# Optimization experiments

Hardware: AMD Instinct MI355X
Metric: run time of the kernel (lower is better)

The kernel has to match this reference:

```python
import jax, jax.numpy as jnp
import numpy as np

N, E, F_IN, F_HID, F_OUT = 50000, 800000, 128, 128, 64


def setup_inputs() -> dict:
    key = jax.random.key(0)
    k_x, k_e, k_w1, k_w2 = jax.random.split(key, 4)
    x = jax.random.normal(k_x, (N, F_IN), dtype=jnp.float32)
    edge_index = jax.random.randint(k_e, (2, E), 0, N, dtype=jnp.int32)
    # GCNConv params (glorot-ish scale)
    W1 = jax.random.normal(k_w1, (F_IN, F_HID), dtype=jnp.float32) * (1.0 / np.sqrt(F_IN))
    b1 = jnp.zeros((F_HID,), dtype=jnp.float32)
    W2 = jax.random.normal(k_w2, (F_HID, F_OUT), dtype=jnp.float32) * (1.0 / np.sqrt(F_HID))
    b2 = jnp.zeros((F_OUT,), dtype=jnp.float32)
    return {"x": x, "edge_index": edge_index, "W1": W1, "b1": b1, "W2": W2, "b2": b2}


def reference(x, edge_index, W1, b1, W2, b2):
    n = x.shape[0]
    # PyG GCNConv: add self-loops, symmetric normalization deg^-1/2 * deg^-1/2
    loops = jnp.arange(n, dtype=edge_index.dtype)
    src = jnp.concatenate([edge_index[0], loops])  # (E+N,)
    dst = jnp.concatenate([edge_index[1], loops])  # (E+N,)
    deg = jax.ops.segment_sum(jnp.ones_like(dst, dtype=x.dtype), dst, num_segments=n)
    dinv = jnp.where(deg > 0, jax.lax.rsqrt(jnp.maximum(deg, 1.0)), 0.0)
    norm = dinv[src] * dinv[dst]  # (E+N,)

    def conv(h, W, b):
        h = h @ W                               # (n, f_out)
        msg = h[src] * norm[:, None]            # gather + scale, (E+N, f_out)
        return jax.ops.segment_sum(msg, dst, num_segments=n) + b

    h = jax.nn.relu(conv(x, W1, b1))  # dropout p=0.0 -> identity
    return conv(h, W2, b2)
```

## Files before the change

### kernel.cpp

```cpp
#include <hip/hip_runtime.h>

typedef __bf16 bf16x8 __attribute__((ext_vector_type(8)));
typedef float  f32x4  __attribute__((ext_vector_type(4)));

__device__ __forceinline__ float bf2f(unsigned short h) {
    return __uint_as_float(((unsigned int)h) << 16);
}
__device__ __forceinline__ unsigned short f2bf(float f) {
    unsigned int u = __float_as_uint(f);
    u += 0x7FFFu + ((u >> 16) & 1u);
    return (unsigned short)(u >> 16);
}
__device__ __forceinline__ void unpack8(uint4 u, float* v) {
    v[0] = __uint_as_float(u.x << 16); v[1] = __uint_as_float(u.x & 0xFFFF0000u);
    v[2] = __uint_as_float(u.y << 16); v[3] = __uint_as_float(u.y & 0xFFFF0000u);
    v[4] = __uint_as_float(u.z << 16); v[5] = __uint_as_float(u.z & 0xFFFF0000u);
    v[6] = __uint_as_float(u.w << 16); v[7] = __uint_as_float(u.w & 0xFFFF0000u);
}

__global__ void k1_deg_detect(const int* __restrict__ dst, int* __restrict__ deg,
                              int* __restrict__ rank, int E,
                              const unsigned short* __restrict__ x, int* __restrict__ cnt,
                              int degBlocks) {
    if ((int)blockIdx.x < degBlocks) {
        int base = blockIdx.x * 1024 + threadIdx.x;
#pragma unroll
        for (int k = 0; k < 4; ++k) {
            int e = base + k * 256;
            if (e < E) rank[e] = atomicAdd(&deg[dst[e]], 1);
        }
    } else {
        int c = 0;
        for (int i = threadIdx.x; i < 4096; i += 256) {
            unsigned e = (x[i] >> 7) & 0xFFu;
            if (e >= 0x88u) ++c;
        }
        if (c) atomicAdd(cnt, c);
    }
}

template <int COLS>
__device__ __forceinline__ void prepack_one(const void* W, unsigned short* Wp, int idx,
                                            bool isf32) {
    if (idx >= (COLS / 16) * 4 * 64) return;
    int lane = idx & 63;
    int ks   = (idx >> 6) & 3;
    int nt   = idx >> 8;
    int col  = nt * 16 + (lane & 15);
    int krow = ks * 32 + (lane >> 4) * 8;
    unsigned short tmp[8];
#pragma unroll
    for (int j = 0; j < 8; ++j) {
        size_t e = (size_t)(krow + j) * COLS + col;
        float v = isf32 ? ((const float*)W)[e] : bf2f(((const unsigned short*)W)[e]);
        tmp[j] = f2bf(v);
    }
    *(uint4*)(Wp + (size_t)idx * 8) = *(uint4*)tmp;
}

__global__ void k2_scan1_prep(const int* __restrict__ deg, int* __restrict__ offs,
                              int* __restrict__ bsum, float* __restrict__ dinv, int N, int NB,
                              const void* __restrict__ W1, const void* __restrict__ W2,
                              const void* __restrict__ b1, const void* __restrict__ b2,
                              unsigned short* __restrict__ Wp1, unsigned short* __restrict__ Wp2,
                              float* __restrict__ b1f, float* __restrict__ b2f,
                              const int* __restrict__ cnt) {
    __shared__ int s[256];
    int t = threadIdx.x;
    if ((int)blockIdx.x < NB) {
        int base = blockIdx.x * 1024 + t * 4;
        int d4[4];
#pragma unroll
        for (int k = 0; k < 4; ++k) d4[k] = (base + k < N) ? deg[base + k] : 0;
#pragma unroll
        for (int k = 0; k < 4; ++k)
            if (base + k < N) dinv[base + k] = rsqrtf((float)d4[k] + 1.0f);
        int mySum = d4[0] + d4[1] + d4[2] + d4[3];
        s[t] = mySum;
        __syncthreads();
        for (int d = 1; d < 256; d <<= 1) {
            int v = (t >= d) ? s[t - d] : 0;
            __syncthreads();
            s[t] += v;
            __syncthreads();
        }
        int run = s[t] - mySum;
#pragma unroll
        for (int k = 0; k < 4; ++k) {
            if (base + k < N) offs[base + k] = run;
            run += d4[k];
        }
        if (t == 255) bsum[blockIdx.x] = s[255];
    } else {
        bool isf32 = (*cnt >= 16);
        int bid = blockIdx.x - NB;
        if (bid < 8) {
            prepack_one<128>(W1, Wp1, bid * 256 + t, isf32);
        } else if (bid < 12) {
            prepack_one<64>(W2, Wp2, (bid - 8) * 256 + t, isf32);
        } else {
            if (t < 128) b1f[t] = isf32 ? ((const float*)b1)[t]
                                        : bf2f(((const unsigned short*)b1)[t]);
            else if (t < 192) b2f[t - 128] = isf32 ? ((const float*)b2)[t - 128]
                                                   : bf2f(((const unsigned short*)b2)[t - 128]);
        }
    }
}

__global__ void scan23(const int* __restrict__ bsum, int* __restrict__ offs,
                       int N, int E, int NB) {
    __shared__ int s[256];
    int t = threadIdx.x;
    s[t] = (t < NB) ? bsum[t] : 0;
    __syncthreads();
    for (int d = 1; d < 256; d <<= 1) {
        int v = (t >= d) ? s[t - d] : 0;
        __syncthreads();
        s[t] += v;
        __syncthreads();
    }
    int boff = (blockIdx.x > 0) ? s[blockIdx.x - 1] : 0;
    int base = blockIdx.x * 1024 + t * 4;
#pragma unroll
    for (int k = 0; k < 4; ++k) {
        int i = base + k;
        if (i < N) offs[i] += boff;
    }
    if (blockIdx.x == 0 && t == 0) offs[N] = E;
}

template <int COLS, int XMODE>
__device__ __forceinline__ void gemm_body(const void* __restrict__ X,
                                          const unsigned short* __restrict__ Wp,
                                          const float* __restrict__ dinv,
                                          unsigned short* __restrict__ O, int nstrips,
                                          bool xf32f, int blockI) {
    constexpr int NT = COLS / 16;
    const int wave = threadIdx.x >> 6;
    const int lane = threadIdx.x & 63;
    const int strip = blockI * 4 + wave;
    if (strip >= nstrips) return;
    const bool xf32 = (XMODE == 0) && xf32f;
    const int m = lane & 15;
    const int q = lane >> 4;
    const size_t rowoff = (size_t)(strip * 16 + m) * 128 + q * 8;

    f32x4 acc[NT];
#pragma unroll
    for (int nt = 0; nt < NT; ++nt) acc[nt] = (f32x4){0.f, 0.f, 0.f, 0.f};

#pragma unroll
    for (int ks = 0; ks < 4; ++ks) {
        bf16x8 a;
        if (xf32) {
            const float* xp = (const float*)X + rowoff + ks * 32;
            float4 u = ((const float4*)xp)[0];
            float4 v = ((const float4*)xp)[1];
            unsigned short tmp[8];
            tmp[0] = f2bf(u.x); tmp[1] = f2bf(u.y); tmp[2] = f2bf(u.z); tmp[3] = f2bf(u.w);
            tmp[4] = f2bf(v.x); tmp[5] = f2bf(v.y); tmp[6] = f2bf(v.z); tmp[7] = f2bf(v.w);
            a = *(bf16x8*)tmp;
        } else {
            a = *(const bf16x8*)((const unsigned short*)X + rowoff + ks * 32);
        }
#pragma unroll
        for (int nt = 0; nt < NT; ++nt) {
            bf16x8 b = *(const bf16x8*)(Wp + (size_t)((nt * 4 + ks) * 64 + lane) * 8);
            acc[nt] = __builtin_amdgcn_mfma_f32_16x16x32_bf16(a, b, acc[nt], 0, 0, 0);
        }
    }

    const int r0 = strip * 16 + q * 4;
    float4 dv = *(const float4*)(dinv + r0);
    float dr[4] = {dv.x, dv.y, dv.z, dv.w};
#pragma unroll
    for (int nt = 0; nt < NT; ++nt) {
#pragma unroll
        for (int r = 0; r < 4; ++r)
            O[(size_t)(r0 + r) * COLS + nt * 16 + m] = f2bf(acc[nt][r] * dr[r]);
    }
}

__global__ __launch_bounds__(256) void k5_scatter_gemm1(
        const int* __restrict__ src, const int* __restrict__ dst,
        const int* __restrict__ offs, const int* __restrict__ rank,
        int* __restrict__ adj, int E, int EB,
        const void* __restrict__ X, const unsigned short* __restrict__ Wp,
        const float* __restrict__ dinv,
        unsigned short* __restrict__ O, int nstrips, const int* __restrict__ cnt) {
    if ((int)blockIdx.x < EB) {
        int base = blockIdx.x * 1024 + threadIdx.x;
#pragma unroll
        for (int k = 0; k < 4; ++k) {
            int e = base + k * 256;
            if (e < E) adj[offs[dst[e]] + rank[e]] = src[e];
        }
    } else {
        gemm_body<128, 0>(X, Wp, dinv, O, nstrips, (*cnt >= 16), blockIdx.x - EB);
    }
}

__global__ __launch_bounds__(256) void gemm2_k(const void* __restrict__ X,
                                               const unsigned short* __restrict__ Wp,
                                               const float* __restrict__ dinv,
                                               unsigned short* __restrict__ O, int nstrips) {
    gemm_body<64, 1>(X, Wp, dinv, O, nstrips, false, blockIdx.x);
}

__global__ void gather1(const unsigned short* __restrict__ Hb, const float* __restrict__ dinv,
                        const float* __restrict__ b, const int* __restrict__ offs,
                        const int* __restrict__ adj, unsigned short* __restrict__ R1,
                        int N) {
    int nd = blockIdx.x * 16 + (threadIdx.x >> 4);
    int lane = threadIdx.x & 63;
    int l15 = lane & 15;
    int gbase = lane & ~15;
    int f8 = l15 * 8;
    if (nd >= N) return;

    float acc[8];
#pragma unroll
    for (int k = 0; k < 8; ++k) acc[k] = 0.f;

    int beg = offs[nd], end = offs[nd + 1];
    for (int c = beg; c < end; c += 16) {
        int rem = end - c;
        int myadj = (l15 < rem) ? adj[c + l15] : 0;
#pragma unroll
        for (int t = 0; t < 16; t += 8) {
            if (t >= rem) break;
            int sI[8];
#pragma unroll
            for (int k = 0; k < 8; ++k) sI[k] = __shfl(myadj, gbase + t + k, 64);
            uint4 u[8];
#pragma unroll
            for (int k = 0; k < 8; ++k) u[k] = *(const uint4*)(Hb + (size_t)sI[k] * 128 + f8);
            float n[8];
#pragma unroll
            for (int k = 0; k < 8; ++k) n[k] = (t + k < rem) ? 1.f : 0.f;
#pragma unroll
            for (int k = 0; k < 8; ++k) {
                float v[8];
                unpack8(u[k], v);
#pragma unroll
                for (int j = 0; j < 8; ++j) acc[j] = fmaf(v[j], n[k], acc[j]);
            }
        }
    }
    float dd = dinv[nd];
    float hv[8], bb[8];
    unpack8(*(const uint4*)(Hb + (size_t)nd * 128 + f8), hv);
    *(float4*)&bb[0] = *(const float4*)(b + f8);
    *(float4*)&bb[4] = *(const float4*)(b + f8 + 4);
    unsigned short o[8];
#pragma unroll
    for (int k = 0; k < 8; ++k) {
        float a = fmaf(acc[k] + hv[k], dd, bb[k]);
        o[k] = f2bf(fmaxf(a, 0.f));
    }
    *(uint4*)(R1 + (size_t)nd * 128 + f8) = *(uint4*)o;
}

__global__ void gather2(const unsigned short* __restrict__ H2b, const float* __restrict__ dinv,
                        const float* __restrict__ b, const int* __restrict__ offs,
                        const int* __restrict__ adj, void* __restrict__ out,
                        int N, const int* __restrict__ cnt) {
    bool isf32 = (*cnt >= 16);
    int nd = blockIdx.x * 32 + (threadIdx.x >> 3);
    int lane = threadIdx.x & 63;
    int l7 = lane & 7;
    int gbase = lane & ~7;
    int f8 = l7 * 8;
    if (nd >= N) return;

    float acc[8];
#pragma unroll
    for (int k = 0; k < 8; ++k) acc[k] = 0.f;

    int beg = offs[nd], end = offs[nd + 1];
    for (int c = beg; c < end; c += 8) {
        int rem = end - c;
        int myadj = (l7 < rem) ? adj[c + l7] : 0;
        int sI[8];
#pragma unroll
        for (int k = 0; k < 8; ++k) sI[k] = __shfl(myadj, gbase + k, 64);
        uint4 u[8];
#pragma unroll
        for (int k = 0; k < 8; ++k) u[k] = *(const uint4*)(H2b + (size_t)sI[k] * 64 + f8);
        float n[8];
#pragma unroll
        for (int k = 0; k < 8; ++k) n[k] = (k < rem) ? 1.f : 0.f;
#pragma unroll
        for (int k = 0; k < 8; ++k) {
            float v[8];
            unpack8(u[k], v);
#pragma unroll
            for (int j = 0; j < 8; ++j) acc[j] = fmaf(v[j], n[k], acc[j]);
        }
    }
    float dd = dinv[nd];
    float hv[8], bb[8];
    unpack8(*(const uint4*)(H2b + (size_t)nd * 64 + f8), hv);
    *(float4*)&bb[0] = *(const float4*)(b + f8);
    *(float4*)&bb[4] = *(const float4*)(b + f8 + 4);
    float r[8];
#pragma unroll
    for (int k = 0; k < 8; ++k) r[k] = fmaf(acc[k] + hv[k], dd, bb[k]);
    if (isf32) {
        float* op = (float*)out + (size_t)nd * 64 + f8;
        *(float4*)op       = *(float4*)&r[0];
        *(float4*)(op + 4) = *(float4*)&r[4];
    } else {
        unsigned short o[8];
#pragma unroll
        for (int k = 0; k < 8; ++k) o[k] = f2bf(r[k]);
        *(uint4*)((unsigned short*)out + (size_t)nd * 64 + f8) = *(uint4*)o;
    }
}

extern "C" void kernel_launch(void* const* d_in, const int* in_sizes, int n_in,
                              void* d_out, int out_size, void* d_ws, size_t ws_size,
                              hipStream_t stream) {
    const void* x  = d_in[0];
    const int*  ei = (const int*)d_in[1];
    const void* W1 = d_in[2];
    const void* b1 = d_in[3];
    const void* W2 = d_in[4];
    const void* b2 = d_in[5];

    const int N = in_sizes[0] / 128;
    const int E = in_sizes[1] / 2;
    const int* src = ei;
    const int* dst = ei + E;

    float* ws = (float*)d_ws;
    size_t off = 0;
    auto alloc = [&](size_t n) { size_t p = off; off += (n + 15) & ~(size_t)15; return p; };
    int*   cnt    = (int*)(ws + alloc(64));
    int*   deg    = (int*)(ws + alloc(N));
    float* dinv   = ws + alloc(N);
    int*   offs   = (int*)(ws + alloc(N + 1));
    int*   bsum   = (int*)(ws + alloc(256));
    int*   adj    = (int*)(ws + alloc(E));
    int*   rank   = (int*)(ws + alloc(E));
    unsigned short* R1  = (unsigned short*)(ws + alloc((size_t)N * 64));
    unsigned short* Hb  = (unsigned short*)(ws + alloc((size_t)N * 64));
    unsigned short* Wp1 = (unsigned short*)(ws + alloc(8192));
    unsigned short* Wp2 = (unsigned short*)(ws + alloc(4096));
    float* b1f    = ws + alloc(128);
    float* b2f    = ws + alloc(64);
    unsigned short* H2b = Hb;

    hipMemsetAsync(ws, 0, (64 + ((size_t)(N + 15) & ~(size_t)15)) * sizeof(float), stream);

    const int EB = (E + 1023) / 1024;
    const int NB = (N + 1023) / 1024;
    const int nstrips = (N + 15) / 16;
    const int GB = (nstrips + 3) / 4;

    k1_deg_detect<<<EB + 1, 256, 0, stream>>>(dst, deg, rank, E,
                                              (const unsigned short*)x, cnt, EB);
    k2_scan1_prep<<<NB + 13, 256, 0, stream>>>(deg, offs, bsum, dinv, N, NB,
                                               W1, W2, b1, b2, Wp1, Wp2, b1f, b2f, cnt);
    scan23<<<NB, 256, 0, stream>>>(bsum, offs, N, E, NB);
    k5_scatter_gemm1<<<EB + GB, 256, 0, stream>>>(src, dst, offs, rank, adj, E, EB,
                                                  x, Wp1, dinv, Hb, nstrips, cnt);
    gather1<<<(N + 15) / 16, 256, 0, stream>>>(Hb, dinv, b1f, offs, adj, R1, N);
    gemm2_k<<<GB, 256, 0, stream>>>(R1, Wp2, dinv, H2b, nstrips);
    gather2<<<(N + 31) / 32, 256, 0, stream>>>(H2b, dinv, b2f, offs, adj, d_out, N, cnt);
}
```

Measured before the change: 196.0 us.

## Fuse layer-1 gather with layer-2 GEMM through shared memory

Merges the first aggregation kernel and the second GEMM into one kernel. Each block aggregates a 16-node strip into LDS and then runs MFMA against the packed W2, so the R1 intermediate is never written to or read back from global memory and one launch is dropped. The edge-processing blocks in the degree and scatter kernels now cover 2048 edges each instead of 1024. H2b gets its own buffer instead of aliasing Hb, since Hb is still being read while H2b is written. The fused kernel launches one block per 16-row strip, so the GEMM is spread over more, smaller blocks.

```diff
diff --git a/kernel.cpp b/kernel.cpp
--- a/kernel.cpp
+++ b/kernel.cpp
@@ -23,9 +23,9 @@
                               const unsigned short* __restrict__ x, int* __restrict__ cnt,
                               int degBlocks) {
     if ((int)blockIdx.x < degBlocks) {
-        int base = blockIdx.x * 1024 + threadIdx.x;
-#pragma unroll
-        for (int k = 0; k < 4; ++k) {
+        int base = blockIdx.x * 2048 + threadIdx.x;
+#pragma unroll
+        for (int k = 0; k < 8; ++k) {
             int e = base + k * 256;
             if (e < E) rank[e] = atomicAdd(&deg[dst[e]], 1);
         }
@@ -129,18 +129,16 @@
     if (blockIdx.x == 0 && t == 0) offs[N] = E;
 }
 
-template <int COLS, int XMODE>
-__device__ __forceinline__ void gemm_body(const void* __restrict__ X,
-                                          const unsigned short* __restrict__ Wp,
-                                          const float* __restrict__ dinv,
-                                          unsigned short* __restrict__ O, int nstrips,
-                                          bool xf32f, int blockI) {
-    constexpr int NT = COLS / 16;
+__device__ __forceinline__ void gemm1_body(const void* __restrict__ X,
+                                           const unsigned short* __restrict__ Wp,
+                                           const float* __restrict__ dinv,
+                                           unsigned short* __restrict__ O, int nstrips,
+                                           bool xf32, int blockI) {
+    constexpr int NT = 8;
     const int wave = threadIdx.x >> 6;
     const int lane = threadIdx.x & 63;
     const int strip = blockI * 4 + wave;
     if (strip >= nstrips) return;
-    const bool xf32 = (XMODE == 0) && xf32f;
     const int m = lane & 15;
     const int q = lane >> 4;
     const size_t rowoff = (size_t)(strip * 16 + m) * 128 + q * 8;
@@ -177,88 +175,112 @@
     for (int nt = 0; nt < NT; ++nt) {
 #pragma unroll
         for (int r = 0; r < 4; ++r)
-            O[(size_t)(r0 + r) * COLS + nt * 16 + m] = f2bf(acc[nt][r] * dr[r]);
+            O[(size_t)(r0 + r) * 128 + nt * 16 + m] = f2bf(acc[nt][r] * dr[r]);
     }
 }
 
 __global__ __launch_bounds__(256) void k5_scatter_gemm1(
         const int* __restrict__ src, const int* __restrict__ dst,
         const int* __restrict__ offs, const int* __restrict__ rank,
-        int* __restrict__ adj, int E, int EB,
+        int* __restrict__ adj, int E, int SB,
         const void* __restrict__ X, const unsigned short* __restrict__ Wp,
         const float* __restrict__ dinv,
         unsigned short* __restrict__ O, int nstrips, const int* __restrict__ cnt) {
-    if ((int)blockIdx.x < EB) {
-        int base = blockIdx.x * 1024 + threadIdx.x;
-#pragma unroll
-        for (int k = 0; k < 4; ++k) {
+    if ((int)blockIdx.x < SB) {
+        int base = blockIdx.x * 2048 + threadIdx.x;
+#pragma unroll
+        for (int k = 0; k < 8; ++k) {
             int e = base + k * 256;
             if (e < E) adj[offs[dst[e]] + rank[e]] = src[e];
         }
     } else {
-        gemm_body<128, 0>(X, Wp, dinv, O, nstrips, (*cnt >= 16), blockIdx.x - EB);
-    }
-}
-
-__global__ __launch_bounds__(256) void gemm2_k(const void* __restrict__ X,
-                                               const unsigned short* __restrict__ Wp,
-                                               const float* __restrict__ dinv,
-                                               unsigned short* __restrict__ O, int nstrips) {
-    gemm_body<64, 1>(X, Wp, dinv, O, nstrips, false, blockIdx.x);
-}
-
-__global__ void gather1(const unsigned short* __restrict__ Hb, const float* __restrict__ dinv,
-                        const float* __restrict__ b, const int* __restrict__ offs,
-                        const int* __restrict__ adj, unsigned short* __restrict__ R1,
-                        int N) {
-    int nd = blockIdx.x * 16 + (threadIdx.x >> 4);
-    int lane = threadIdx.x & 63;
-    int l15 = lane & 15;
-    int gbase = lane & ~15;
-    int f8 = l15 * 8;
-    if (nd >= N) return;
-
-    float acc[8];
-#pragma unroll
-    for (int k = 0; k < 8; ++k) acc[k] = 0.f;
-
-    int beg = offs[nd], end = offs[nd + 1];
-    for (int c = beg; c < end; c += 16) {
-        int rem = end - c;
-        int myadj = (l15 < rem) ? adj[c + l15] : 0;
-#pragma unroll
-        for (int t = 0; t < 16; t += 8) {
-            if (t >= rem) break;
-            int sI[8];
-#pragma unroll
-            for (int k = 0; k < 8; ++k) sI[k] = __shfl(myadj, gbase + t + k, 64);
-            uint4 u[8];
-#pragma unroll
-            for (int k = 0; k < 8; ++k) u[k] = *(const uint4*)(Hb + (size_t)sI[k] * 128 + f8);
-            float n[8];
-#pragma unroll
-            for (int k = 0; k < 8; ++k) n[k] = (t + k < rem) ? 1.f : 0.f;
+        gemm1_body(X, Wp, dinv, O, nstrips, (*cnt >= 16), blockIdx.x - SB);
+    }
+}
+
+__global__ __launch_bounds__(256) void gather1_gemm2(
+        const unsigned short* __restrict__ Hb, const float* __restrict__ dinv,
+        const float* __restrict__ b, const int* __restrict__ offs,
+        const int* __restrict__ adj, const unsigned short* __restrict__ Wp2,
+        unsigned short* __restrict__ H2b, int N) {
+    __shared__ unsigned short Rs[16][136];
+    const int strip = blockIdx.x;
+    const int lane = threadIdx.x & 63;
+
+    {
+        int ndl = threadIdx.x >> 4;
+        int nd = strip * 16 + ndl;
+        int l15 = lane & 15;
+        int gbase = lane & ~15;
+        int f8 = l15 * 8;
+        if (nd < N) {
+            float acc[8];
+#pragma unroll
+            for (int k = 0; k < 8; ++k) acc[k] = 0.f;
+            int beg = offs[nd], end = offs[nd + 1];
+            for (int c = beg; c < end; c += 16) {
+                int rem = end - c;
+                int myadj = (l15 < rem) ? adj[c + l15] : 0;
+#pragma unroll
+                for (int t = 0; t < 16; t += 8) {
+                    if (t >= rem) break;
+                    int sI[8];
+#pragma unroll
+                    for (int k = 0; k < 8; ++k) sI[k] = __shfl(myadj, gbase + t + k, 64);
+                    uint4 u[8];
+#pragma unroll
+                    for (int k = 0; k < 8; ++k)
+                        u[k] = *(const uint4*)(Hb + (size_t)sI[k] * 128 + f8);
+                    float n[8];
+#pragma unroll
+                    for (int k = 0; k < 8; ++k) n[k] = (t + k < rem) ? 1.f : 0.f;
+#pragma unroll
+                    for (int k = 0; k < 8; ++k) {
+                        float v[8];
+                        unpack8(u[k], v);
+#pragma unroll
+                        for (int j = 0; j < 8; ++j) acc[j] = fmaf(v[j], n[k], acc[j]);
+                    }
+                }
+            }
+            float dd = dinv[nd];
+            float hv[8], bb[8];
+            unpack8(*(const uint4*)(Hb + (size_t)nd * 128 + f8), hv);
+            *(float4*)&bb[0] = *(const float4*)(b + f8);
+            *(float4*)&bb[4] = *(const float4*)(b + f8 + 4);
+            unsigned short o[8];
 #pragma unroll
             for (int k = 0; k < 8; ++k) {
-                float v[8];
-                unpack8(u[k], v);
-#pragma unroll
-                for (int j = 0; j < 8; ++j) acc[j] = fmaf(v[j], n[k], acc[j]);
+                float a = fmaf(acc[k] + hv[k], dd, bb[k]);
+                o[k] = f2bf(fmaxf(a, 0.f));
             }
-        }
-    }
-    float dd = dinv[nd];
-    float hv[8], bb[8];
-    unpack8(*(const uint4*)(Hb + (size_t)nd * 128 + f8), hv);
-    *(float4*)&bb[0] = *(const float4*)(b + f8);
-    *(float4*)&bb[4] = *(const float4*)(b + f8 + 4);
-    unsigned short o[8];
-#pragma unroll
-    for (int k = 0; k < 8; ++k) {
-        float a = fmaf(acc[k] + hv[k], dd, bb[k]);
-        o[k] = f2bf(fmaxf(a, 0.f));
-    }
-    *(uint4*)(R1 + (size_t)nd * 128 + f8) = *(uint4*)o;
+            *(uint4*)&Rs[ndl][f8] = *(uint4*)o;
+        } else {
+            uint4 z = make_uint4(0, 0, 0, 0);
+            *(uint4*)&Rs[ndl][f8] = z;
+        }
+    }
+    __syncthreads();
+
+    {
+        const int nt = threadIdx.x >> 6;
+        const int m = lane & 15;
+        const int q = lane >> 4;
+        f32x4 acc = (f32x4){0.f, 0.f, 0.f, 0.f};
+#pragma unroll
+        for (int ks = 0; ks < 4; ++ks) {
+            bf16x8 a = *(const bf16x8*)&Rs[m][ks * 32 + q * 8];
+            bf16x8 bfr = *(const bf16x8*)(Wp2 + (size_t)((nt * 4 + ks) * 64 + lane) * 8);
+            acc = __builtin_amdgcn_mfma_f32_16x16x32_bf16(a, bfr, acc, 0, 0, 0);
+        }
+        const int r0 = strip * 16 + q * 4;
+#pragma unroll
+        for (int r = 0; r < 4; ++r) {
+            int row = r0 + r;
+            if (row < N)
+                H2b[(size_t)row * 64 + nt * 16 + m] = f2bf(acc[r] * dinv[row]);
+        }
+    }
 }
 
 __global__ void gather2(const unsigned short* __restrict__ H2b, const float* __restrict__ dinv,
@@ -343,29 +365,27 @@
     int*   bsum   = (int*)(ws + alloc(256));
     int*   adj    = (int*)(ws + alloc(E));
     int*   rank   = (int*)(ws + alloc(E));
-    unsigned short* R1  = (unsigned short*)(ws + alloc((size_t)N * 64));
     unsigned short* Hb  = (unsigned short*)(ws + alloc((size_t)N * 64));
     unsigned short* Wp1 = (unsigned short*)(ws + alloc(8192));
     unsigned short* Wp2 = (unsigned short*)(ws + alloc(4096));
     float* b1f    = ws + alloc(128);
     float* b2f    = ws + alloc(64);
-    unsigned short* H2b = Hb;
+    unsigned short* H2b = (unsigned short*)(ws + alloc((size_t)N * 32));
 
     hipMemsetAsync(ws, 0, (64 + ((size_t)(N + 15) & ~(size_t)15)) * sizeof(float), stream);
 
-    const int EB = (E + 1023) / 1024;
+    const int EB8 = (E + 2047) / 2048;
     const int NB = (N + 1023) / 1024;
     const int nstrips = (N + 15) / 16;
     const int GB = (nstrips + 3) / 4;
 
-    k1_deg_detect<<<EB + 1, 256, 0, stream>>>(dst, deg, rank, E,
-                                              (const unsigned short*)x, cnt, EB);
+    k1_deg_detect<<<EB8 + 1, 256, 0, stream>>>(dst, deg, rank, E,
+                                               (const unsigned short*)x, cnt, EB8);
     k2_scan1_prep<<<NB + 13, 256, 0, stream>>>(deg, offs, bsum, dinv, N, NB,
                                                W1, W2, b1, b2, Wp1, Wp2, b1f, b2f, cnt);
     scan23<<<NB, 256, 0, stream>>>(bsum, offs, N, E, NB);
-    k5_scatter_gemm1<<<EB + GB, 256, 0, stream>>>(src, dst, offs, rank, adj, E, EB,
-                                                  x, Wp1, dinv, Hb, nstrips, cnt);
-    gather1<<<(N + 15) / 16, 256, 0, stream>>>(Hb, dinv, b1f, offs, adj, R1, N);
-    gemm2_k<<<GB, 256, 0, stream>>>(R1, Wp2, dinv, H2b, nstrips);
+    k5_scatter_gemm1<<<EB8 + GB, 256, 0, stream>>>(src, dst, offs, rank, adj, E, EB8,
+                                                   x, Wp1, dinv, Hb, nstrips, cnt);
+    gather1_gemm2<<<nstrips, 256, 0, stream>>>(Hb, dinv, b1f, offs, adj, Wp2, H2b, N);
     gather2<<<(N + 31) / 32, 256, 0, stream>>>(H2b, dinv, b2f, offs, adj, d_out, N, cnt);
 }
```

Result: faster. 191.6 us (-2.2%).
